# Kernel optimization log

Measured on AMD Instinct MI355X. Metric: run time of the kernel, lower is better.

## Reference

```python
import jax, jax.numpy as jnp
import numpy as np

EMBED_DIM = 1024
HEAD_DIM = 64


def setup_inputs() -> dict:
    key = jax.random.key(0)
    ks = jax.random.split(key, 7)
    s_in = EMBED_DIM ** -0.5  # torch Linear default init scale
    x = jax.random.normal(ks[0], (4, 4096, EMBED_DIM), dtype=jnp.float32)
    Wk = jax.random.uniform(ks[1], (HEAD_DIM, EMBED_DIM), jnp.float32, -s_in, s_in)
    bk = jax.random.uniform(ks[2], (HEAD_DIM,), jnp.float32, -s_in, s_in)
    Wq = jax.random.uniform(ks[3], (HEAD_DIM, EMBED_DIM), jnp.float32, -s_in, s_in)
    bq = jax.random.uniform(ks[4], (HEAD_DIM,), jnp.float32, -s_in, s_in)
    Wv = jax.random.uniform(ks[5], (HEAD_DIM, EMBED_DIM), jnp.float32, -s_in, s_in)
    bv = jax.random.uniform(ks[6], (HEAD_DIM,), jnp.float32, -s_in, s_in)
    return {"x": x, "Wq": Wq, "bq": bq, "Wk": Wk, "bk": bk, "Wv": Wv, "bv": bv}


def reference(x, Wq, bq, Wk, bk, Wv, bv):
    # torch Linear: y = x @ W.T + b
    q = jnp.einsum('btc,dc->btd', x, Wq) + bq  # [B,T,D]
    k = jnp.einsum('btc,dc->btd', x, Wk) + bk
    v = jnp.einsum('btc,dc->btd', x, Wv) + bv
    scale = HEAD_DIM ** -0.5
    # NOTE: original divides by scale (multiplies by sqrt(head_dim)) -- faithful
    scores = jnp.einsum('btd,bsd->bts', q, k) / scale  # [B,T,T]
    attn_weights = jax.nn.softmax(scores, axis=-1)
    return jnp.einsum('bts,bsd->btd', attn_weights, v)
```

## Files before the change

kernel.cpp:

```cpp
#include <hip/hip_runtime.h>

#define BATCH 4
#define SEQ   4096
#define CDIM  1024
#define DDIM  64
#define NROW  (BATCH * SEQ)
#define NSPL  8
#define SEG   (NROW * DDIM)

typedef _Float16 f16;
typedef _Float16 f16x8 __attribute__((ext_vector_type(8)));
typedef _Float16 f16x4 __attribute__((ext_vector_type(4)));
typedef __fp16   h16x2 __attribute__((ext_vector_type(2)));
typedef float    f32x4 __attribute__((ext_vector_type(4)));

#define MFMA32(a, b, c) __builtin_amdgcn_mfma_f32_16x16x32_f16((a), (b), (c), 0, 0, 0)
#define MFMA16(a, b, c) __builtin_amdgcn_mfma_f32_16x16x16f16((a), (b), (c), 0, 0, 0)

#define GLDS(g, l)                                                            \
  __builtin_amdgcn_global_load_lds((const __attribute__((address_space(1))) void*)(g), \
                                   (__attribute__((address_space(3))) void*)(l), 16, 0, 0)

#define QSCALE 11.5415603f

__device__ inline f16x8 cvt8(f32x4 a, f32x4 b) {
  h16x2 p0 = __builtin_amdgcn_cvt_pkrtz(a[0], a[1]);
  h16x2 p1 = __builtin_amdgcn_cvt_pkrtz(a[2], a[3]);
  h16x2 p2 = __builtin_amdgcn_cvt_pkrtz(b[0], b[1]);
  h16x2 p3 = __builtin_amdgcn_cvt_pkrtz(b[2], b[3]);
  f16x8 r;
  r[0] = p0[0]; r[1] = p0[1]; r[2] = p1[0]; r[3] = p1[1];
  r[4] = p2[0]; r[5] = p2[1]; r[6] = p3[0]; r[7] = p3[1];
  return r;
}

__device__ inline f16x4 cvt4(float a, float b, float c, float d) {
  h16x2 lo = __builtin_amdgcn_cvt_pkrtz(a, b);
  h16x2 hi = __builtin_amdgcn_cvt_pkrtz(c, d);
  f16x4 r;
  r[0] = lo[0]; r[1] = lo[1]; r[2] = hi[0]; r[3] = hi[1];
  return r;
}

__global__ __launch_bounds__(256) void prep_w_kernel(const float* __restrict__ Wq,
                                                     const float* __restrict__ Wk,
                                                     const float* __restrict__ Wv,
                                                     f16* __restrict__ wf2) {
  const int t = blockIdx.x * 256 + threadIdx.x;
  const int lane = t & 63;
  const int s = t >> 6;
  const int mt = s >> 5, ck = s & 31;
  const int mat = mt >> 2, tile = mt & 3;
  const int n = lane & 15, quad = lane >> 4;
  const float* W = (mat == 0) ? Wq : (mat == 1) ? Wk : Wv;
  const float* src = W + (size_t)(tile * 16 + n) * CDIM + ck * 32 + quad * 8;
  const f32x4 a = *(const f32x4*)src;
  const f32x4 b = *(const f32x4*)(src + 4);
  *(f16x8*)(wf2 + (size_t)t * 8) = cvt8(a, b);
}

__global__ __launch_bounds__(256, 2) void proj_kernel(const float* __restrict__ x,
                                                      const f16* __restrict__ wf2,
                                                      const float* __restrict__ bq,
                                                      const float* __restrict__ bk,
                                                      const float* __restrict__ bv,
                                                      f16* __restrict__ qs,
                                                      f16* __restrict__ ks,
                                                      f16* __restrict__ vc) {
  const int tid = threadIdx.x, lane = tid & 63, w = tid >> 6;
  const int n = lane & 15, quad = lane >> 4;
  const int row16 = blockIdx.x * 32 + (w & 1) * 16;
  const int mtb = (w >> 1) * 6;

  const float* xp = x + (size_t)(row16 + n) * CDIM + quad * 8;
  f16x8 xf[32];
#pragma unroll
  for (int ck = 0; ck < 32; ++ck) {
    const f32x4 a = *(const f32x4*)(xp + ck * 32);
    const f32x4 c = *(const f32x4*)(xp + ck * 32 + 4);
    xf[ck] = cvt8(a, c);
  }

  const f16* wl = wf2 + (size_t)lane * 8;
#pragma unroll
  for (int p = 0; p < 2; ++p) {
    const int m0 = mtb + p * 3;
    const f16* wb = wl + (size_t)m0 * 16384;
    f32x4 acc[3];
#pragma unroll
    for (int i = 0; i < 3; ++i) acc[i] = (f32x4){0.f, 0.f, 0.f, 0.f};
#pragma unroll
    for (int ck = 0; ck < 32; ++ck) {
      const f16x8 w0 = *(const f16x8*)(wb + ck * 512);
      const f16x8 w1 = *(const f16x8*)(wb + 16384 + ck * 512);
      const f16x8 w2 = *(const f16x8*)(wb + 32768 + ck * 512);
      acc[0] = MFMA32(xf[ck], w0, acc[0]);
      acc[1] = MFMA32(xf[ck], w1, acc[1]);
      acc[2] = MFMA32(xf[ck], w2, acc[2]);
    }

    const int r0 = row16 + quad * 4;
#pragma unroll
    for (int i2 = 0; i2 < 3; ++i2) {
      const int mt = m0 + i2;
      const int mat = mt >> 2, tile = mt & 3;
      const int d = tile * 16 + n;
      const f32x4 aa = acc[i2];
      if (mat == 0) {
        const float bi = bq[d];
#pragma unroll
        for (int r = 0; r < 4; ++r)
          qs[(size_t)(r0 + r) * DDIM + d] = (f16)((aa[r] + bi) * QSCALE);
      } else if (mat == 1) {
        const float bi = bk[d];
#pragma unroll
        for (int r = 0; r < 4; ++r) {
          const int tt = r0 + r;
          const int col = ((((d >> 3) ^ (tt & 7)) << 3) | (d & 7));
          ks[(size_t)tt * DDIM + col] = (f16)(aa[r] + bi);
        }
      } else {
        const float bi = bv[d];
        const int bb = r0 >> 12;
        const int tl = r0 & (SEQ - 1);
        const int ck2 = tl >> 6;
        const int bsw = (((tl & 63) >> 2) ^ n) << 2;
        *(f16x4*)(vc + ((size_t)(bb * 64 + ck2) * 64 + d) * 64 + bsw) =
            cvt4(aa[0] + bi, aa[1] + bi, aa[2] + bi, aa[3] + bi);
      }
    }
  }
}

template <int NSPLIT>
__global__ __launch_bounds__(256, 4) void attn_kernel(const f16* __restrict__ qs,
                                                      const f16* __restrict__ ks,
                                                      const f16* __restrict__ vc,
                                                      float* __restrict__ outp,
                                                      f16* __restrict__ pacc,
                                                      float* __restrict__ pm,
                                                      float* __restrict__ pl) {
  __shared__ __attribute__((aligned(16))) f16 lk[2][4096];
  __shared__ __attribute__((aligned(16))) f16 lv[2][4096];
  const int tid = threadIdx.x, lane = tid & 63, w = tid >> 6;
  const int n = lane & 15, quad = lane >> 4;
  const int split = blockIdx.x % NSPLIT;
  const int rowblk = blockIdx.x / NSPLIT;
  const int row0 = rowblk * 128 + w * 32;
  const int bb = row0 >> 12;
  const int kbase = split * (SEQ / NSPLIT);
  const int kc0 = kbase >> 6;
  const int NC = SEQ / NSPLIT / 64;

  const f16* ksb = ks + (size_t)bb * SEQ * DDIM;
  const f16* vcb = vc + (size_t)bb * 64 * 4096;

  auto issue = [&](int c, int buf) {
#pragma unroll
    for (int i = 0; i < 2; ++i) {
      const int id = 2 * w + i;
      GLDS(ksb + (size_t)(kbase + c * 64) * 64 + id * 512 + lane * 8, &lk[buf][id * 512]);
      GLDS(vcb + (size_t)(kc0 + c) * 4096 + id * 512 + lane * 8, &lv[buf][id * 512]);
    }
  };

  f16x8 qf[2][2];
#pragma unroll
  for (int g = 0; g < 2; ++g)
#pragma unroll
    for (int hh = 0; hh < 2; ++hh)
      qf[g][hh] = *(const f16x8*)(qs + (size_t)(row0 + g * 16 + n) * DDIM + hh * 32 + quad * 8);

  const int kswz = (quad ^ (n & 7)) << 3;
  int vswz[4];
#pragma unroll
  for (int st = 0; st < 4; ++st) vswz[st] = ((((st << 2) | quad) ^ n) << 2);

  f32x4 acc[2][4];
  float m[2] = {-1e30f, -1e30f}, ll[2] = {0.f, 0.f};
#pragma unroll
  for (int g = 0; g < 2; ++g)
#pragma unroll
    for (int t = 0; t < 4; ++t) acc[g][t] = (f32x4){0.f, 0.f, 0.f, 0.f};

  issue(0, 0);
  for (int c = 0; c < NC; ++c) {
    const int b = c & 1;
    __syncthreads();
    if (c + 1 < NC) issue(c + 1, b ^ 1);

    f32x4 s[2][4];
#pragma unroll
    for (int st = 0; st < 4; ++st) {
      const f16* lkr = &lk[b][(st * 16 + n) * 64];
      const f16x8 klo = *(const f16x8*)(lkr + kswz);
      const f16x8 khi = *(const f16x8*)(lkr + (kswz ^ 32));
#pragma unroll
      for (int g = 0; g < 2; ++g) {
        f32x4 z = (f32x4){0.f, 0.f, 0.f, 0.f};
        z = MFMA32(klo, qf[g][0], z);
        s[g][st] = MFMA32(khi, qf[g][1], z);
      }
    }

    f16x4 pq[2][4];
#pragma unroll
    for (int g = 0; g < 2; ++g) {
      f32x4 mx;
#pragma unroll
      for (int r = 0; r < 4; ++r)
        mx[r] = fmaxf(fmaxf(s[g][0][r], s[g][1][r]), fmaxf(s[g][2][r], s[g][3][r]));
      float mloc = fmaxf(fmaxf(mx[0], mx[1]), fmaxf(mx[2], mx[3]));
      mloc = fmaxf(mloc, __shfl_xor(mloc, 16));
      mloc = fmaxf(mloc, __shfl_xor(mloc, 32));
      const float mnew = fmaxf(m[g], mloc);
      const float alpha = __builtin_amdgcn_exp2f(m[g] - mnew);
      m[g] = mnew;
      float psum = 0.f;
#pragma unroll
      for (int st = 0; st < 4; ++st) {
        f32x4 p;
#pragma unroll
        for (int r = 0; r < 4; ++r) p[r] = __builtin_amdgcn_exp2f(s[g][st][r] - mnew);
        psum += (p[0] + p[1]) + (p[2] + p[3]);
        pq[g][st] = cvt4(p[0], p[1], p[2], p[3]);
      }
      ll[g] = ll[g] * alpha + psum;
#pragma unroll
      for (int t = 0; t < 4; ++t) acc[g][t] *= alpha;
    }

#pragma unroll
    for (int dt = 0; dt < 4; ++dt) {
      const f16* lvr = &lv[b][(dt * 16 + n) * 64];
#pragma unroll
      for (int st = 0; st < 4; ++st) {
        const f16x4 va = *(const f16x4*)(lvr + vswz[st]);
        acc[0][dt] = MFMA16(va, pq[0][st], acc[0][dt]);
        acc[1][dt] = MFMA16(va, pq[1][st], acc[1][dt]);
      }
    }
  }

  float lred[2];
#pragma unroll
  for (int g = 0; g < 2; ++g) {
    float l = ll[g];
    l += __shfl_xor(l, 16);
    l += __shfl_xor(l, 32);
    lred[g] = l;
  }

  if (NSPLIT == 1) {
#pragma unroll
    for (int g = 0; g < 2; ++g) {
      const float inv = 1.0f / lred[g];
      const int q = row0 + g * 16 + n;
#pragma unroll
      for (int t = 0; t < 4; ++t) {
        f32x4 o = acc[g][t];
#pragma unroll
        for (int r = 0; r < 4; ++r) o[r] *= inv;
        *(f32x4*)(outp + (size_t)q * DDIM + t * 16 + quad * 4) = o;
      }
    }
  } else {
#pragma unroll
    for (int g = 0; g < 2; ++g) {
      const int q = row0 + g * 16 + n;
#pragma unroll
      for (int t = 0; t < 4; ++t)
        *(f16x4*)(pacc + ((size_t)split * NROW + q) * DDIM + t * 16 + quad * 4) =
            cvt4(acc[g][t][0], acc[g][t][1], acc[g][t][2], acc[g][t][3]);
      if (quad == 0) {
        pm[split * NROW + q] = m[g];
        pl[split * NROW + q] = lred[g];
      }
    }
  }
}

template <int NSPLIT>
__global__ __launch_bounds__(256) void combine_kernel(const f16* __restrict__ pacc,
                                                      const float* __restrict__ pm,
                                                      const float* __restrict__ pl,
                                                      float* __restrict__ out) {
  const int idx = blockIdx.x * 256 + threadIdx.x;
  const int row = idx >> 4;
  const int c = (idx & 15) * 4;
  float mm = pm[row];
#pragma unroll
  for (int s = 1; s < NSPLIT; ++s) mm = fmaxf(mm, pm[s * NROW + row]);
  float L = 0.f;
  f32x4 o = (f32x4){0.f, 0.f, 0.f, 0.f};
#pragma unroll
  for (int s = 0; s < NSPLIT; ++s) {
    const float e = __builtin_amdgcn_exp2f(pm[s * NROW + row] - mm);
    L += pl[s * NROW + row] * e;
    const f16x4 a = *(const f16x4*)(pacc + ((size_t)s * NROW + row) * DDIM + c);
#pragma unroll
    for (int j = 0; j < 4; ++j) o[j] += (float)a[j] * e;
  }
  const float inv = 1.0f / L;
#pragma unroll
  for (int j = 0; j < 4; ++j) o[j] *= inv;
  *(f32x4*)(out + (size_t)row * DDIM + c) = o;
}

extern "C" void kernel_launch(void* const* d_in, const int* in_sizes, int n_in,
                              void* d_out, int out_size, void* d_ws, size_t ws_size,
                              hipStream_t stream) {
  const float* x  = (const float*)d_in[0];
  const float* Wq = (const float*)d_in[1];
  const float* bq = (const float*)d_in[2];
  const float* Wk = (const float*)d_in[3];
  const float* bk = (const float*)d_in[4];
  const float* Wv = (const float*)d_in[5];
  const float* bv = (const float*)d_in[6];
  float* out = (float*)d_out;

  f16* wf2 = (f16*)d_ws;
  f16* qs = wf2 + 3 * 65536;
  f16* ks = qs + (size_t)SEG;
  f16* vc = ks + (size_t)SEG;
  f16* pacc = vc + (size_t)SEG;
  float* pm = (float*)(pacc + (size_t)NSPL * SEG);
  float* pl = pm + (size_t)NSPL * NROW;
  const size_t need = (size_t)((char*)(pl + (size_t)NSPL * NROW) - (char*)d_ws);

  prep_w_kernel<<<dim3(96), dim3(256), 0, stream>>>(Wq, Wk, Wv, wf2);
  proj_kernel<<<dim3(512), dim3(256), 0, stream>>>(x, wf2, bq, bk, bv, qs, ks, vc);

  if (ws_size >= need) {
    attn_kernel<NSPL><<<dim3(128 * NSPL), dim3(256), 0, stream>>>(qs, ks, vc, nullptr, pacc, pm, pl);
    combine_kernel<NSPL><<<dim3(NROW * 16 / 256), dim3(256), 0, stream>>>(pacc, pm, pl, out);
  } else {
    attn_kernel<1><<<dim3(128), dim3(256), 0, stream>>>(qs, ks, vc, out, nullptr, nullptr, nullptr);
  }
}
```

Before: 165.4 us.

## Stream x tiles through double-buffered LDS in projection kernel

The projection kernel now computes 16 rows per block instead of 32, with each of the four waves handling 3 output tiles. It no longer keeps the whole 1024-wide x row in registers as f16. Instead it stages x in 128-column chunks into LDS with async global_load_lds, using double buffering and an XOR swizzle, and converts to f16 just before each MFMA. This cuts register pressure, allowing 4 blocks per CU and a grid of 1024 blocks, and overlaps the x loads with MFMA work. In exchange it adds LDS traffic, a barrier per chunk, and more total weight loads because each block now covers fewer rows.

```diff
diff --git a/kernel.cpp b/kernel.cpp
--- a/kernel.cpp
+++ b/kernel.cpp
@@ -59,7 +59,7 @@
   *(f16x8*)(wf2 + (size_t)t * 8) = cvt8(a, b);
 }
 
-__global__ __launch_bounds__(256, 2) void proj_kernel(const float* __restrict__ x,
+__global__ __launch_bounds__(256, 4) void proj_kernel(const float* __restrict__ x,
                                                       const f16* __restrict__ wf2,
                                                       const float* __restrict__ bq,
                                                       const float* __restrict__ bk,
@@ -67,67 +67,84 @@
                                                       f16* __restrict__ qs,
                                                       f16* __restrict__ ks,
                                                       f16* __restrict__ vc) {
+  __shared__ __attribute__((aligned(16))) char lx[2][8192];
   const int tid = threadIdx.x, lane = tid & 63, w = tid >> 6;
   const int n = lane & 15, quad = lane >> 4;
-  const int row16 = blockIdx.x * 32 + (w & 1) * 16;
-  const int mtb = (w >> 1) * 6;
-
-  const float* xp = x + (size_t)(row16 + n) * CDIM + quad * 8;
-  f16x8 xf[32];
-#pragma unroll
-  for (int ck = 0; ck < 32; ++ck) {
-    const f32x4 a = *(const f32x4*)(xp + ck * 32);
-    const f32x4 c = *(const f32x4*)(xp + ck * 32 + 4);
-    xf[ck] = cvt8(a, c);
-  }
-
-  const f16* wl = wf2 + (size_t)lane * 8;
-#pragma unroll
-  for (int p = 0; p < 2; ++p) {
-    const int m0 = mtb + p * 3;
-    const f16* wb = wl + (size_t)m0 * 16384;
-    f32x4 acc[3];
-#pragma unroll
-    for (int i = 0; i < 3; ++i) acc[i] = (f32x4){0.f, 0.f, 0.f, 0.f};
-#pragma unroll
-    for (int ck = 0; ck < 32; ++ck) {
-      const f16x8 w0 = *(const f16x8*)(wb + ck * 512);
-      const f16x8 w1 = *(const f16x8*)(wb + 16384 + ck * 512);
-      const f16x8 w2 = *(const f16x8*)(wb + 32768 + ck * 512);
-      acc[0] = MFMA32(xf[ck], w0, acc[0]);
-      acc[1] = MFMA32(xf[ck], w1, acc[1]);
-      acc[2] = MFMA32(xf[ck], w2, acc[2]);
-    }
-
-    const int r0 = row16 + quad * 4;
-#pragma unroll
-    for (int i2 = 0; i2 < 3; ++i2) {
-      const int mt = m0 + i2;
-      const int mat = mt >> 2, tile = mt & 3;
-      const int d = tile * 16 + n;
-      const f32x4 aa = acc[i2];
-      if (mat == 0) {
-        const float bi = bq[d];
-#pragma unroll
-        for (int r = 0; r < 4; ++r)
-          qs[(size_t)(r0 + r) * DDIM + d] = (f16)((aa[r] + bi) * QSCALE);
-      } else if (mat == 1) {
-        const float bi = bk[d];
-#pragma unroll
-        for (int r = 0; r < 4; ++r) {
-          const int tt = r0 + r;
-          const int col = ((((d >> 3) ^ (tt & 7)) << 3) | (d & 7));
-          ks[(size_t)tt * DDIM + col] = (f16)(aa[r] + bi);
-        }
-      } else {
-        const float bi = bv[d];
-        const int bb = r0 >> 12;
-        const int tl = r0 & (SEQ - 1);
-        const int ck2 = tl >> 6;
-        const int bsw = (((tl & 63) >> 2) ^ n) << 2;
-        *(f16x4*)(vc + ((size_t)(bb * 64 + ck2) * 64 + d) * 64 + bsw) =
-            cvt4(aa[0] + bi, aa[1] + bi, aa[2] + bi, aa[3] + bi);
-      }
+  const int rowbase = blockIdx.x * 16;
+  const int mtb = 3 * w;
+
+  const float* xsrc[2];
+#pragma unroll
+  for (int j = 0; j < 2; ++j) {
+    const int id = 2 * w + j;
+    const int r = id * 2 + (lane >> 5);
+    const int c = (lane & 31) ^ r;
+    xsrc[j] = x + (size_t)(rowbase + r) * CDIM + c * 4;
+  }
+
+  auto issue = [&](int ck, int b) {
+    char* base = &lx[b][0];
+#pragma unroll
+    for (int j = 0; j < 2; ++j)
+      GLDS(xsrc[j] + ck * 128, base + (2 * w + j) * 1024);
+  };
+
+  const f16* wl = wf2 + (size_t)mtb * 16384 + lane * 8;
+
+  f32x4 acc[3];
+#pragma unroll
+  for (int i = 0; i < 3; ++i) acc[i] = (f32x4){0.f, 0.f, 0.f, 0.f};
+
+  issue(0, 0);
+  for (int ck = 0; ck < 8; ++ck) {
+    const int b = ck & 1;
+    __syncthreads();
+    if (ck + 1 < 8) issue(ck + 1, b ^ 1);
+    const char* xb = &lx[b][0] + n * 512;
+#pragma unroll
+    for (int kk = 0; kk < 4; ++kk) {
+      const int c1 = kk * 8 + quad * 2;
+      const f32x4 xa = *(const f32x4*)(xb + ((c1 ^ n) << 4));
+      const f32x4 xc = *(const f32x4*)(xb + (((c1 + 1) ^ n) << 4));
+      const f16x8 af = cvt8(xa, xc);
+      const f16* wq = wl + (size_t)(ck * 4 + kk) * 512;
+      const f16x8 w0 = *(const f16x8*)(wq);
+      const f16x8 w1 = *(const f16x8*)(wq + 16384);
+      const f16x8 w2 = *(const f16x8*)(wq + 32768);
+      acc[0] = MFMA32(af, w0, acc[0]);
+      acc[1] = MFMA32(af, w1, acc[1]);
+      acc[2] = MFMA32(af, w2, acc[2]);
+    }
+  }
+
+  const int r0 = rowbase + quad * 4;
+#pragma unroll
+  for (int i2 = 0; i2 < 3; ++i2) {
+    const int mt = mtb + i2;
+    const int mat = mt >> 2, tile = mt & 3;
+    const int d = tile * 16 + n;
+    const f32x4 aa = acc[i2];
+    if (mat == 0) {
+      const float bi = bq[d];
+#pragma unroll
+      for (int r = 0; r < 4; ++r)
+        qs[(size_t)(r0 + r) * DDIM + d] = (f16)((aa[r] + bi) * QSCALE);
+    } else if (mat == 1) {
+      const float bi = bk[d];
+#pragma unroll
+      for (int r = 0; r < 4; ++r) {
+        const int tt = r0 + r;
+        const int col = ((((d >> 3) ^ (tt & 7)) << 3) | (d & 7));
+        ks[(size_t)tt * DDIM + col] = (f16)(aa[r] + bi);
+      }
+    } else {
+      const float bi = bv[d];
+      const int bb = r0 >> 12;
+      const int tl = r0 & (SEQ - 1);
+      const int ck2 = tl >> 6;
+      const int bsw = (((tl & 63) >> 2) ^ n) << 2;
+      *(f16x4*)(vc + ((size_t)(bb * 64 + ck2) * 64 + d) * 64 + bsw) =
+          cvt4(aa[0] + bi, aa[1] + bi, aa[2] + bi, aa[3] + bi);
     }
   }
 }
@@ -329,7 +346,7 @@
   const size_t need = (size_t)((char*)(pl + (size_t)NSPL * NROW) - (char*)d_ws);
 
   prep_w_kernel<<<dim3(96), dim3(256), 0, stream>>>(Wq, Wk, Wv, wf2);
-  proj_kernel<<<dim3(512), dim3(256), 0, stream>>>(x, wf2, bq, bk, bv, qs, ks, vc);
+  proj_kernel<<<dim3(NROW / 16), dim3(256), 0, stream>>>(x, wf2, bq, bk, bv, qs, ks, vc);
 
   if (ws_size >= need) {
     attn_kernel<NSPL><<<dim3(128 * NSPL), dim3(256), 0, stream>>>(qs, ks, vc, nullptr, pacc, pm, pl);
```

Measured after the change: 154.5 us. 1.07x faster.
